# Optimization experiments

Measured on AMD Instinct MI355X. Metric: run time of the kernel, lower is better.

The kernel has to match this reference:

```python
import jax, jax.numpy as jnp
import numpy as np
import math

B, H_IM, W_IM, HDIM, HEADS, PS = 16, 56, 56, 512, 8, 7


def setup_inputs() -> dict:
    key = jax.random.key(0)
    ks = jax.random.split(key, 4)
    x = jax.random.normal(ks[0], (B, H_IM * W_IM, HDIM), jnp.float32)
    mask = jnp.zeros((1, 1, H_IM, W_IM), jnp.bool_)
    Wqkv = jax.random.normal(ks[1], (HDIM, 3 * HDIM), jnp.float32) * 0.02
    Wproj = jax.random.normal(ks[2], (HDIM, HDIM), jnp.float32) * 0.02
    bproj = jnp.zeros((HDIM,), jnp.float32)
    rel_bias = jax.random.normal(ks[3], (HEADS, PS * PS, PS * PS), jnp.float32) * 0.02
    return {"x": x, "mask": mask, "Wqkv": Wqkv, "Wproj": Wproj,
            "bproj": bproj, "rel_bias": rel_bias, "H": H_IM, "W": W_IM}


def reference(x, mask, Wqkv, Wproj, bproj, rel_bias, H, W):
    b = x.shape[0]
    ps, g, hd = PS, HEADS, HDIM
    dh = hd // g
    scale = dh ** (-0.5)

    qkv = x @ Wqkv                                   # [b, H*W, 3*hd]
    qkv = qkv.reshape(b, H, W, 3 * hd)
    pad_b = int(math.ceil(H / ps)) * ps - H
    pad_r = int(math.ceil(W / ps)) * ps - W
    qkv = jnp.pad(qkv, ((0, 0), (0, pad_b), (0, pad_r), (0, 0)))
    kmask = jnp.pad(mask, ((0, 0), (0, 0), (0, pad_b), (0, pad_r)), constant_values=True)
    Hp, Wp = H + pad_b, W + pad_r
    sh, sw = Hp // ps, Wp // ps
    K, P = ps * ps, sh * sw

    # patchify: b (sh kh) (sw kw) c -> b (kh kw) (sh sw) c
    qkv = qkv.reshape(b, sh, ps, sw, ps, 3 * hd).transpose(0, 2, 4, 1, 3, 5).reshape(b, K, P, 3 * hd)
    kmask = kmask.reshape(1, 1, sh, ps, sw, ps).transpose(0, 1, 3, 5, 2, 4).reshape(1, 1, K, P)

    qkv = qkv.reshape(b, K, P, 3, g, dh)
    q, k, v = qkv[:, :, :, 0], qkv[:, :, :, 1], qkv[:, :, :, 2]  # each [b, K, P, g, dh]

    attn = jnp.einsum('bqpgc,bkpgc->bgqkp', q, k)    # [b, g, K, K, P]
    attn = (attn + rel_bias[None, :, :, :, None]) * scale
    m = kmask[:, None]                                # [1, 1, 1, K, P]
    attn = jnp.where(m, -jnp.inf, attn)
    attn = jax.nn.softmax(attn, axis=-2)              # softmax over key positions within window
    attn = jnp.where(m, 0.0, attn)

    out = jnp.einsum('bgqkp,bkpgc->bqpgc', attn, v)
    out = out.reshape(b, K, P, hd)
    # un-patchify: b (kh kw) (sh sw) c -> b (sh kh) (sw kw) c
    out = out.reshape(b, ps, ps, sh, sw, hd).transpose(0, 3, 1, 4, 2, 5).reshape(b, Hp, Wp, hd)
    out = out[:, :H, :W, :].reshape(b, H * W, hd)
    return out @ Wproj + bproj
```

## Files before the change

### kernel.cpp

```cpp
#include <hip/hip_runtime.h>
#include <hip/hip_bf16.h>

using bf16 = __hip_bfloat16;
using bf16x8 = __attribute__((ext_vector_type(8))) short;
using f32x4  = __attribute__((ext_vector_type(4))) float;

#define B_    16
#define HIM   56
#define WIM   56
#define HD    512
#define NHEAD 8
#define DH    64
#define NTOK  (HIM*WIM)
#define M_    (B_*NTOK)
#define K49   49

__device__ __forceinline__ void gload_lds16(const void* g, void* l) {
  __builtin_amdgcn_global_load_lds(
      (__attribute__((address_space(1))) const void*)g,
      (__attribute__((address_space(3))) void*)l, 16, 0, 0);
}

__global__ __launch_bounds__(256) void cvt_x_kernel(const float* __restrict__ in,
                                                    bf16* __restrict__ out) {
  size_t i = ((size_t)blockIdx.x * 256 + threadIdx.x) * 8;
  float4 a = *(const float4*)(in + i);
  float4 b = *(const float4*)(in + i + 4);
  union { uint4 v; bf16 h[8]; } o;
  o.h[0] = __float2bfloat16(a.x); o.h[1] = __float2bfloat16(a.y);
  o.h[2] = __float2bfloat16(a.z); o.h[3] = __float2bfloat16(a.w);
  o.h[4] = __float2bfloat16(b.x); o.h[5] = __float2bfloat16(b.y);
  o.h[6] = __float2bfloat16(b.z); o.h[7] = __float2bfloat16(b.w);
  *(uint4*)(out + i) = o.v;
}

__global__ __launch_bounds__(256) void cvt_transpose_kernel(const float* __restrict__ in,
                                                            bf16* __restrict__ out,
                                                            int K, int N) {
  int idx = blockIdx.x * 256 + threadIdx.x;
  int k = idx / N, n = idx - k * N;
  out[(size_t)n * K + k] = __float2bfloat16(in[idx]);
}

template<int N, bool OUT_BF16, bool BIAS>
__global__ __launch_bounds__(512, 2) void gemm256_kernel(
    const bf16* __restrict__ A,
    const bf16* __restrict__ Bt,
    void* __restrict__ Cp,
    const float* __restrict__ bias,
    int NBX)
{
  constexpr int K  = 512;
  constexpr int NK = K / 32;
  __shared__ alignas(16) bf16 lds[2][4][256 * 32];
  const int tid  = threadIdx.x;
  const int lane = tid & 63, wid = tid >> 6;
  const int l15  = lane & 15, kq = lane >> 4;
  const int wm   = wid >> 2,  wn = wid & 3;
  const int cpx = gridDim.x >> 3;
  const int wg  = (blockIdx.x & 7) * cpx + (blockIdx.x >> 3);
  const int by  = wg / NBX, bx = wg - by * NBX;
  const long arow0 = (long)by * 256;
  const long bcol0 = (long)bx * 256;

  auto stageHalf = [&](int ab, int j) {
    const bf16* g = (ab ? Bt + bcol0 * K : A + arow0 * K) + j * 32;
    bf16* lbase = &lds[ab][j & 3][0];
#pragma unroll
    for (int c = 0; c < 2; ++c) {
      int s   = c * 512 + tid;
      int row = s >> 2, sl = s & 3;
      int gs  = sl ^ ((row >> 1) & 3);
      gload_lds16((const char*)(g + (long)row * K) + gs * 16,
                  lbase + (c * 512 + wid * 64) * 8);
    }
  };

  f32x4 acc[8][4] = {};

#define KSLICE(SL, VMSTR, DOSTAGE, JSTAGE) {                                            \
    asm volatile("s_waitcnt vmcnt(" VMSTR ")" ::: "memory");                            \
    __builtin_amdgcn_s_barrier();                                                       \
    bf16x8 af[8], bb[4];                                                                \
    _Pragma("unroll")                                                                   \
    for (int mt = 0; mt < 8; ++mt) {                                                    \
      int row = wm * 128 + mt * 16 + l15;                                               \
      af[mt] = *(const bf16x8*)&lds[0][SL][row * 32 + ((kq ^ ((row >> 1) & 3)) << 3)];  \
    }                                                                                   \
    _Pragma("unroll")                                                                   \
    for (int nt = 0; nt < 4; ++nt) {                                                    \
      int row = wn * 64 + nt * 16 + l15;                                                \
      bb[nt] = *(const bf16x8*)&lds[1][SL][row * 32 + ((kq ^ ((row >> 1) & 3)) << 3)];  \
    }                                                                                   \
    if (DOSTAGE) { stageHalf(0, JSTAGE); stageHalf(1, JSTAGE); }                        \
    __builtin_amdgcn_s_setprio(1);                                                      \
    _Pragma("unroll")                                                                   \
    for (int mt = 0; mt < 8; ++mt)                                                      \
      _Pragma("unroll")                                                                 \
      for (int nt = 0; nt < 4; ++nt)                                                    \
        acc[mt][nt] = __builtin_amdgcn_mfma_f32_16x16x32_bf16(bb[nt], af[mt],           \
                                                              acc[mt][nt], 0, 0, 0);    \
    __builtin_amdgcn_s_setprio(0);                                                      \
  }

  stageHalf(0, 0); stageHalf(1, 0);
  stageHalf(0, 1); stageHalf(1, 1);
  stageHalf(0, 2); stageHalf(1, 2);

#pragma unroll 1
  for (int jo = 0; jo < NK - 4; jo += 4) {
    KSLICE(0, "8", true, jo + 3);
    KSLICE(1, "8", true, jo + 4);
    KSLICE(2, "8", true, jo + 5);
    KSLICE(3, "8", true, jo + 6);
  }
  KSLICE(0, "8", true,  15);
  KSLICE(1, "8", false, 0);
  KSLICE(2, "4", false, 0);
  KSLICE(3, "0", false, 0);
#undef KSLICE

  const long crow0 = arow0 + wm * 128;
  const long ccol0 = bcol0 + wn * 64 + kq * 4;
#pragma unroll
  for (int mt = 0; mt < 8; ++mt) {
    long row = crow0 + mt * 16 + l15;
#pragma unroll
    for (int nt = 0; nt < 4; ++nt) {
      long col = ccol0 + nt * 16;
      if (OUT_BF16) {
        union { unsigned long long u; unsigned short h[4]; } pk;
#pragma unroll
        for (int r = 0; r < 4; ++r) {
          bf16 hh = __float2bfloat16(acc[mt][nt][r]);
          pk.h[r] = *(unsigned short*)&hh;
        }
        __builtin_nontemporal_store(pk.u,
            (unsigned long long*)((bf16*)Cp + row * N + col));
      } else {
        f32x4 o = acc[mt][nt];
        if (BIAS) {
          o[0] += bias[col];     o[1] += bias[col + 1];
          o[2] += bias[col + 2]; o[3] += bias[col + 3];
        }
        __builtin_nontemporal_store(o, (f32x4*)((float*)Cp + row * N + col));
      }
    }
  }
}

__global__ __launch_bounds__(256) void attn_win_kernel(
    const bf16* __restrict__ qkv, const float* __restrict__ rb, bf16* __restrict__ outa)
{
  __shared__ alignas(16) bf16 Qs[64 * 72];
  __shared__ alignas(16) bf16 Ks[64 * 72];
  __shared__ alignas(16) bf16 Vt[64 * 72];
  __shared__ alignas(16) bf16 Ps[64 * 72];
  const int tid = threadIdx.x, lane = tid & 63, wid = tid >> 6;
  const int p = blockIdx.x, g = blockIdx.y, b = blockIdx.z;
  const int sh = p >> 3, sw = p & 7;
  const size_t nb = (size_t)b * NTOK;
  const int c8 = (tid & 7) * 8;

#pragma unroll
  for (int it = 0; it < 2; ++it) {
    int t = (tid >> 3) + it * 32;
    uint4 vq = {0, 0, 0, 0}, vk = vq, vv = vq;
    if (t < K49) {
      int ph = t / 7, pw = t - ph * 7;
      int n = (sh * 7 + ph) * WIM + sw * 7 + pw;
      const bf16* src = qkv + (nb + n) * 1536 + g * 64 + c8;
      vq = *(const uint4*)(src);
      vk = *(const uint4*)(src + 512);
      vv = *(const uint4*)(src + 1024);
    }
    *(uint4*)&Qs[t * 72 + c8] = vq;
    *(uint4*)&Ks[t * 72 + c8] = vk;
    union { uint4 u; unsigned short s[8]; } uv; uv.u = vv;
    unsigned short* vt16 = (unsigned short*)Vt;
#pragma unroll
    for (int e = 0; e < 8; ++e) vt16[(c8 + e) * 72 + t] = uv.s[e];
  }
  __syncthreads();

  const int l15 = lane & 15, kq = lane >> 4;
  bf16x8 aq[2];
#pragma unroll
  for (int kk = 0; kk < 2; ++kk)
    aq[kk] = *(const bf16x8*)&Qs[(wid * 16 + l15) * 72 + kk * 32 + kq * 8];
  float sv[4][4];
#pragma unroll
  for (int ct = 0; ct < 4; ++ct) {
    f32x4 acc = {0.f, 0.f, 0.f, 0.f};
#pragma unroll
    for (int kk = 0; kk < 2; ++kk) {
      bf16x8 bk = *(const bf16x8*)&Ks[(ct * 16 + l15) * 72 + kk * 32 + kq * 8];
      acc = __builtin_amdgcn_mfma_f32_16x16x32_bf16(aq[kk], bk, acc, 0, 0, 0);
    }
    int kcol = ct * 16 + l15;
#pragma unroll
    for (int r = 0; r < 4; ++r) {
      int q = wid * 16 + kq * 4 + r;
      float bias = (q < K49 && kcol < K49) ? rb[((size_t)g * K49 + q) * K49 + kcol] : 0.f;
      float v = (acc[r] + bias) * 0.125f;
      sv[ct][r] = (kcol < K49) ? v : -1e30f;
    }
  }
#pragma unroll
  for (int r = 0; r < 4; ++r) {
    float m = fmaxf(fmaxf(sv[0][r], sv[1][r]), fmaxf(sv[2][r], sv[3][r]));
#pragma unroll
    for (int d = 1; d < 16; d <<= 1) m = fmaxf(m, __shfl_xor(m, d));
    float e0 = __expf(sv[0][r] - m), e1 = __expf(sv[1][r] - m);
    float e2 = __expf(sv[2][r] - m), e3 = __expf(sv[3][r] - m);
    float s = e0 + e1 + e2 + e3;
#pragma unroll
    for (int d = 1; d < 16; d <<= 1) s += __shfl_xor(s, d);
    float inv = 1.0f / s;
    int q = wid * 16 + kq * 4 + r;
    Ps[q * 72 +  0 + l15] = __float2bfloat16(e0 * inv);
    Ps[q * 72 + 16 + l15] = __float2bfloat16(e1 * inv);
    Ps[q * 72 + 32 + l15] = __float2bfloat16(e2 * inv);
    Ps[q * 72 + 48 + l15] = __float2bfloat16(e3 * inv);
  }
  __syncthreads();
  bf16x8 ap[2];
#pragma unroll
  for (int kk = 0; kk < 2; ++kk)
    ap[kk] = *(const bf16x8*)&Ps[(wid * 16 + l15) * 72 + kk * 32 + kq * 8];
#pragma unroll
  for (int ct = 0; ct < 4; ++ct) {
    f32x4 acc = {0.f, 0.f, 0.f, 0.f};
#pragma unroll
    for (int kk = 0; kk < 2; ++kk) {
      bf16x8 bv = *(const bf16x8*)&Vt[(ct * 16 + l15) * 72 + kk * 32 + kq * 8];
      acc = __builtin_amdgcn_mfma_f32_16x16x32_bf16(ap[kk], bv, acc, 0, 0, 0);
    }
#pragma unroll
    for (int r = 0; r < 4; ++r) {
      int q = wid * 16 + kq * 4 + r;
      if (q < K49) {
        int ph = q / 7, pw = q - ph * 7;
        int n = (sh * 7 + ph) * WIM + sw * 7 + pw;
        outa[(nb + n) * HD + g * 64 + ct * 16 + l15] = __float2bfloat16(acc[r]);
      }
    }
  }
}

extern "C" void kernel_launch(void* const* d_in, const int* in_sizes, int n_in,
                              void* d_out, int out_size, void* d_ws, size_t ws_size,
                              hipStream_t stream) {
  (void)in_sizes; (void)n_in; (void)out_size;
  const float* x     = (const float*)d_in[0];
  const float* wqkv  = (const float*)d_in[2];
  const float* wproj = (const float*)d_in[3];
  const float* bproj = (const float*)d_in[4];
  const float* rb    = (const float*)d_in[5];

  char* ws = (char*)d_ws;
  bf16* x_bf    = (bf16*)(ws);
  bf16* wqkv_t  = (bf16*)(ws + 51380224);
  bf16* wproj_t = (bf16*)(ws + 52953088);
  bf16* qkv     = (bf16*)(ws + 53477376);
  bf16* attno   = x_bf;
  float* out    = (float*)d_out;
  if (ws_size < 207618048) return;

  cvt_x_kernel<<<dim3(12544), 256, 0, stream>>>(x, x_bf);
  cvt_transpose_kernel<<<dim3(3072), 256, 0, stream>>>(wqkv, wqkv_t, 512, 1536);
  cvt_transpose_kernel<<<dim3(1024), 256, 0, stream>>>(wproj, wproj_t, 512, 512);
  gemm256_kernel<1536, true, false><<<dim3(1176), 512, 0, stream>>>(
      x_bf, wqkv_t, (void*)qkv, nullptr, 6);
  attn_win_kernel<<<dim3(64, NHEAD, B_), 256, 0, stream>>>(qkv, rb, attno);
  gemm256_kernel<512, false, true><<<dim3(392), 512, 0, stream>>>(
      attno, wproj_t, (void*)out, bproj, 2);
}
```

Baseline: 256.4 us.

## Restructure GEMM K-loop with split staging and B-fragment prefetch; vectorize attention output stores

After: 255.4 us (median of 5 runs). No clear change (-0.4%).

```diff
diff --git a/kernel.cpp b/kernel.cpp
--- a/kernel.cpp
+++ b/kernel.cpp
@@ -43,15 +43,14 @@
 }
 
 template<int N, bool OUT_BF16, bool BIAS>
-__global__ __launch_bounds__(512, 2) void gemm256_kernel(
+__global__ __launch_bounds__(512, 2) void gemm8p_kernel(
     const bf16* __restrict__ A,
     const bf16* __restrict__ Bt,
     void* __restrict__ Cp,
     const float* __restrict__ bias,
     int NBX)
 {
-  constexpr int K  = 512;
-  constexpr int NK = K / 32;
+  constexpr int K = 512;
   __shared__ alignas(16) bf16 lds[2][4][256 * 32];
   const int tid  = threadIdx.x;
   const int lane = tid & 63, wid = tid >> 6;
@@ -65,60 +64,80 @@
 
   auto stageHalf = [&](int ab, int j) {
     const bf16* g = (ab ? Bt + bcol0 * K : A + arow0 * K) + j * 32;
-    bf16* lbase = &lds[ab][j & 3][0];
+    bf16* lb = &lds[ab][j & 3][0];
 #pragma unroll
     for (int c = 0; c < 2; ++c) {
       int s   = c * 512 + tid;
       int row = s >> 2, sl = s & 3;
       int gs  = sl ^ ((row >> 1) & 3);
       gload_lds16((const char*)(g + (long)row * K) + gs * 16,
-                  lbase + (c * 512 + wid * 64) * 8);
+                  lb + (c * 512 + wid * 64) * 8);
     }
   };
+  auto rdA = [&](int slot, int mt) -> bf16x8 {
+    int rr = wm * 128 + mt * 16 + l15;
+    return *(const bf16x8*)&lds[0][slot][rr * 32 + ((kq ^ ((rr >> 1) & 3)) << 3)];
+  };
+  auto rdB = [&](int slot, int nt) -> bf16x8 {
+    int rr = wn * 64 + nt * 16 + l15;
+    return *(const bf16x8*)&lds[1][slot][rr * 32 + ((kq ^ ((rr >> 1) & 3)) << 3)];
+  };
 
   f32x4 acc[8][4] = {};
-
-#define KSLICE(SL, VMSTR, DOSTAGE, JSTAGE) {                                            \
-    asm volatile("s_waitcnt vmcnt(" VMSTR ")" ::: "memory");                            \
-    __builtin_amdgcn_s_barrier();                                                       \
-    bf16x8 af[8], bb[4];                                                                \
-    _Pragma("unroll")                                                                   \
-    for (int mt = 0; mt < 8; ++mt) {                                                    \
-      int row = wm * 128 + mt * 16 + l15;                                               \
-      af[mt] = *(const bf16x8*)&lds[0][SL][row * 32 + ((kq ^ ((row >> 1) & 3)) << 3)];  \
-    }                                                                                   \
-    _Pragma("unroll")                                                                   \
-    for (int nt = 0; nt < 4; ++nt) {                                                    \
-      int row = wn * 64 + nt * 16 + l15;                                                \
-      bb[nt] = *(const bf16x8*)&lds[1][SL][row * 32 + ((kq ^ ((row >> 1) & 3)) << 3)];  \
-    }                                                                                   \
-    if (DOSTAGE) { stageHalf(0, JSTAGE); stageHalf(1, JSTAGE); }                        \
-    __builtin_amdgcn_s_setprio(1);                                                      \
-    _Pragma("unroll")                                                                   \
-    for (int mt = 0; mt < 8; ++mt)                                                      \
-      _Pragma("unroll")                                                                 \
-      for (int nt = 0; nt < 4; ++nt)                                                    \
-        acc[mt][nt] = __builtin_amdgcn_mfma_f32_16x16x32_bf16(bb[nt], af[mt],           \
-                                                              acc[mt][nt], 0, 0, 0);    \
-    __builtin_amdgcn_s_setprio(0);                                                      \
-  }
+  bf16x8 af[8], bfA[4], bfB[4];
 
   stageHalf(0, 0); stageHalf(1, 0);
   stageHalf(0, 1); stageHalf(1, 1);
   stageHalf(0, 2); stageHalf(1, 2);
+  asm volatile("s_waitcnt vmcnt(4)" ::: "memory");
+  __builtin_amdgcn_s_barrier();
+#pragma unroll
+  for (int nt = 0; nt < 4; ++nt) bfA[nt] = rdB(0, nt);
+
+#define KS(SLOT, NSLOT, BFC, BFN, JST, DOST, PRE, VMSTR) {                    \
+    _Pragma("unroll")                                                         \
+    for (int mt = 0; mt < 8; ++mt) af[mt] = rdA(SLOT, mt);                    \
+    if (DOST) stageHalf(0, JST);                                              \
+    __builtin_amdgcn_s_barrier();                                             \
+    __builtin_amdgcn_s_setprio(1);                                            \
+    _Pragma("unroll")                                                         \
+    for (int mt = 0; mt < 8; ++mt) {                                          \
+      acc[mt][0] = __builtin_amdgcn_mfma_f32_16x16x32_bf16(BFC[0], af[mt],    \
+                                                           acc[mt][0], 0,0,0);\
+      acc[mt][1] = __builtin_amdgcn_mfma_f32_16x16x32_bf16(BFC[1], af[mt],    \
+                                                           acc[mt][1], 0,0,0);\
+    }                                                                         \
+    __builtin_amdgcn_s_setprio(0);                                            \
+    if (DOST) stageHalf(1, JST);                                              \
+    __builtin_amdgcn_s_setprio(1);                                            \
+    _Pragma("unroll")                                                         \
+    for (int mt = 0; mt < 8; ++mt) {                                          \
+      acc[mt][2] = __builtin_amdgcn_mfma_f32_16x16x32_bf16(BFC[2], af[mt],    \
+                                                           acc[mt][2], 0,0,0);\
+      acc[mt][3] = __builtin_amdgcn_mfma_f32_16x16x32_bf16(BFC[3], af[mt],    \
+                                                           acc[mt][3], 0,0,0);\
+    }                                                                         \
+    __builtin_amdgcn_s_setprio(0);                                            \
+    if (PRE) {                                                                \
+      _Pragma("unroll")                                                       \
+      for (int nt = 0; nt < 4; ++nt) BFN[nt] = rdB(NSLOT, nt);                \
+    }                                                                         \
+    asm volatile("s_waitcnt vmcnt(" VMSTR ")" ::: "memory");                  \
+    __builtin_amdgcn_s_barrier();                                             \
+  }
 
 #pragma unroll 1
-  for (int jo = 0; jo < NK - 4; jo += 4) {
-    KSLICE(0, "8", true, jo + 3);
-    KSLICE(1, "8", true, jo + 4);
-    KSLICE(2, "8", true, jo + 5);
-    KSLICE(3, "8", true, jo + 6);
-  }
-  KSLICE(0, "8", true,  15);
-  KSLICE(1, "8", false, 0);
-  KSLICE(2, "4", false, 0);
-  KSLICE(3, "0", false, 0);
-#undef KSLICE
+  for (int jo = 0; jo < 12; jo += 4) {
+    KS(0, 1, bfA, bfB, jo + 3, 1, 1, "4");
+    KS(1, 2, bfB, bfA, jo + 4, 1, 1, "4");
+    KS(2, 3, bfA, bfB, jo + 5, 1, 1, "4");
+    KS(3, 0, bfB, bfA, jo + 6, 1, 1, "4");
+  }
+  KS(0, 1, bfA, bfB, 15, 1, 1, "4");
+  KS(1, 2, bfB, bfA, 0,  0, 1, "0");
+  KS(2, 3, bfA, bfB, 0,  0, 1, "0");
+  KS(3, 0, bfB, bfA, 0,  0, 0, "0");
+#undef KS
 
   const long crow0 = arow0 + wm * 128;
   const long ccol0 = bcol0 + wn * 64 + kq * 4;
@@ -228,22 +247,27 @@
 #pragma unroll
   for (int kk = 0; kk < 2; ++kk)
     ap[kk] = *(const bf16x8*)&Ps[(wid * 16 + l15) * 72 + kk * 32 + kq * 8];
-#pragma unroll
-  for (int ct = 0; ct < 4; ++ct) {
-    f32x4 acc = {0.f, 0.f, 0.f, 0.f};
+  f32x4 accO[4] = {};
+#pragma unroll
+  for (int ct = 0; ct < 4; ++ct)
 #pragma unroll
     for (int kk = 0; kk < 2; ++kk) {
       bf16x8 bv = *(const bf16x8*)&Vt[(ct * 16 + l15) * 72 + kk * 32 + kq * 8];
-      acc = __builtin_amdgcn_mfma_f32_16x16x32_bf16(ap[kk], bv, acc, 0, 0, 0);
-    }
-#pragma unroll
-    for (int r = 0; r < 4; ++r) {
-      int q = wid * 16 + kq * 4 + r;
-      if (q < K49) {
-        int ph = q / 7, pw = q - ph * 7;
-        int n = (sh * 7 + ph) * WIM + sw * 7 + pw;
-        outa[(nb + n) * HD + g * 64 + ct * 16 + l15] = __float2bfloat16(acc[r]);
+      accO[ct] = __builtin_amdgcn_mfma_f32_16x16x32_bf16(bv, ap[kk], accO[ct], 0, 0, 0);
+    }
+  int q = wid * 16 + l15;
+  if (q < K49) {
+    int ph = q / 7, pw = q - ph * 7;
+    bf16* dst = outa + (nb + (sh * 7 + ph) * WIM + sw * 7 + pw) * HD + g * 64 + kq * 4;
+#pragma unroll
+    for (int ct = 0; ct < 4; ++ct) {
+      union { unsigned long long u; unsigned short h[4]; } pk;
+#pragma unroll
+      for (int r = 0; r < 4; ++r) {
+        bf16 hh = __float2bfloat16(accO[ct][r]);
+        pk.h[r] = *(unsigned short*)&hh;
       }
+      *(unsigned long long*)(dst + ct * 16) = pk.u;
     }
   }
 }
@@ -270,9 +294,9 @@
   cvt_x_kernel<<<dim3(12544), 256, 0, stream>>>(x, x_bf);
   cvt_transpose_kernel<<<dim3(3072), 256, 0, stream>>>(wqkv, wqkv_t, 512, 1536);
   cvt_transpose_kernel<<<dim3(1024), 256, 0, stream>>>(wproj, wproj_t, 512, 512);
-  gemm256_kernel<1536, true, false><<<dim3(1176), 512, 0, stream>>>(
+  gemm8p_kernel<1536, true, false><<<dim3(1176), 512, 0, stream>>>(
       x_bf, wqkv_t, (void*)qkv, nullptr, 6);
   attn_win_kernel<<<dim3(64, NHEAD, B_), 256, 0, stream>>>(qkv, rb, attno);
-  gemm256_kernel<512, false, true><<<dim3(392), 512, 0, stream>>>(
+  gemm8p_kernel<512, false, true><<<dim3(392), 512, 0, stream>>>(
       attno, wproj_t, (void*)out, bproj, 2);
 }
```
